# Optimization experiments

Measured on AMD Instinct MI355X. Metric: run time of the kernel, lower is better.

The kernel has to match this reference:

```python
import jax, jax.numpy as jnp
import numpy as np

B, L, K, D = 1024, 8, 16, 64
_KSCALE = 1.0 / np.sqrt(K * D)  # keep channel roughly norm-preserving over layers


def setup_inputs() -> dict:
    key = jax.random.key(0)
    k1, k2, k3, k4 = jax.random.split(key, 4)
    state_re = jax.random.normal(k1, (B, D, D), dtype=jnp.float32)
    state_im = jax.random.normal(k2, (B, D, D), dtype=jnp.float32)
    kraus_re = jax.random.normal(k3, (L, K, D, D), dtype=jnp.float32) * _KSCALE
    kraus_im = jax.random.normal(k4, (L, K, D, D), dtype=jnp.float32) * _KSCALE
    return {"state_re": state_re, "state_im": state_im,
            "kraus_re": kraus_re, "kraus_im": kraus_im}


def reference(state_re, state_im, kraus_re, kraus_im):
    # rho: [B, d, d] complex density matrices; kraus: [L, K, d, d]
    rho = (state_re + 1j * state_im).astype(jnp.complex64)
    kraus = (kraus_re + 1j * kraus_im).astype(jnp.complex64)

    def layer_step(rho, Kl):
        # Kl: [K, d, d]. output_state = sum_k  K_k @ rho @ K_k^dagger
        tmp = jnp.einsum('kij,bjl->kbil', Kl, rho)            # K_k @ rho
        rho_new = jnp.einsum('kbil,kml->bim', tmp, Kl.conj())  # (...) @ K_k^dagger, summed over k
        return rho_new, None

    rho, _ = jax.lax.scan(layer_step, rho, kraus)
    # return real/imag stacked as float32: [2, B, d, d]
    return jnp.stack([rho.real, rho.imag])
```

## Files before the change

### kernel.cpp

```cpp
#include <hip/hip_runtime.h>
#include <hip/hip_fp16.h>

#define D 64
#define NKR 16
#define NB 1024
#define NL 8
#define LSTR 72

typedef __attribute__((ext_vector_type(8))) _Float16 half8;
typedef __attribute__((ext_vector_type(16))) float f32x16;
typedef __attribute__((ext_vector_type(4))) int i32x4;

static __device__ __forceinline__ half8 neg8(half8 x) {
    i32x4 u = __builtin_bit_cast(i32x4, x);
    u = u ^ (int)0x80008000;
    return __builtin_bit_cast(half8, u);
}

union Pack4 { _Float16 h[4]; uint2 u; };

__global__ void kconv_kernel(const float* __restrict__ re, const float* __restrict__ im,
                             _Float16* __restrict__ out) {
    int plane = blockIdx.y;
    int idx = blockIdx.x * blockDim.x + threadIdx.x;
    const float* src = plane ? im : re;
    float4 v = ((const float4*)src)[idx];
    int e = idx * 4;
    int lk = e >> 12;
    int rem = e & 4095;
    Pack4 p;
    p.h[0] = (_Float16)v.x; p.h[1] = (_Float16)v.y;
    p.h[2] = (_Float16)v.z; p.h[3] = (_Float16)v.w;
    *(uint2*)(out + ((size_t)lk * 2 + plane) * 4096 + rem) = p.u;
}

__global__ void sconv_kernel(const float* __restrict__ re, const float* __restrict__ im,
                             _Float16* __restrict__ out) {
    __shared__ float tile[64][65];
    int b = blockIdx.x;
    int t = threadIdx.x;
    for (int plane = 0; plane < 2; ++plane) {
        const float* src = (plane ? im : re) + (size_t)b * 4096;
        __syncthreads();
        #pragma unroll
        for (int i = 0; i < 16; ++i) {
            int e = t + 256 * i;
            tile[e >> 6][e & 63] = src[e];
        }
        __syncthreads();
        _Float16* o = out + ((size_t)b * 2 + plane) * 4096;
        #pragma unroll
        for (int i = 0; i < 16; ++i) {
            int e = t + 256 * i;
            o[e] = (_Float16)tile[e & 63][e >> 6];
        }
    }
}

__global__ __launch_bounds__(256, 4) void layer_kernel(
    const _Float16* __restrict__ rho_in,
    _Float16* __restrict__ rho_out,
    float* __restrict__ final_out,
    const _Float16* __restrict__ kraus,
    int last)
{
    __shared__ __align__(16) _Float16 Klds[2][D][LSTR];
    __shared__ __align__(16) _Float16 Trow[2][D][LSTR];

    const int b    = blockIdx.x;
    const int t    = threadIdx.x;
    const int wv   = t >> 6;
    const int lane = t & 63;
    const int l31  = lane & 31;
    const int hl   = lane >> 5;
    const int wr   = wv >> 1;
    const int wc   = wv & 1;

    half8 a1re[4], a1im[4];
    {
        const _Float16* rb = rho_in + (size_t)b * 2 * D * D;
        const int row = 32 * wr + l31;
        #pragma unroll
        for (int ks = 0; ks < 4; ++ks) {
            const int col = 16 * ks + 8 * hl;
            a1re[ks] = *(const half8*)(rb + row * D + col);
            a1im[ks] = *(const half8*)(rb + D * D + row * D + col);
        }
    }

    f32x16 accRe, accIm;
    #pragma unroll
    for (int i = 0; i < 16; ++i) { accRe[i] = 0.f; accIm[i] = 0.f; }

    #pragma unroll 1
    for (int k = 0; k < NKR; ++k) {
        const uint4* kg = (const uint4*)(kraus + (size_t)k * 2 * D * D);
        #pragma unroll
        for (int r = 0; r < 4; ++r) {
            int idx = t + 256 * r;
            int e0  = idx * 8;
            int plane = e0 >> 12;
            int rem   = e0 & 4095;
            *(uint4*)&Klds[plane][rem >> 6][rem & 63] = kg[idx];
        }
        __syncthreads();

        f32x16 dre, dim;
        #pragma unroll
        for (int i = 0; i < 16; ++i) { dre[i] = 0.f; dim[i] = 0.f; }
        #pragma unroll
        for (int ks = 0; ks < 4; ++ks) {
            const int jcol = 16 * ks + 8 * hl;
            half8 bre  = *(const half8*)&Klds[0][32 * wc + l31][jcol];
            half8 bim  = *(const half8*)&Klds[1][32 * wc + l31][jcol];
            half8 bimn = neg8(bim);
            dre = __builtin_amdgcn_mfma_f32_32x32x16_f16(a1re[ks], bre,  dre, 0, 0, 0);
            dre = __builtin_amdgcn_mfma_f32_32x32x16_f16(a1im[ks], bimn, dre, 0, 0, 0);
            dim = __builtin_amdgcn_mfma_f32_32x32x16_f16(a1re[ks], bim,  dim, 0, 0, 0);
            dim = __builtin_amdgcn_mfma_f32_32x32x16_f16(a1im[ks], bre,  dim, 0, 0, 0);
        }
        {
            const int i = 32 * wc + l31;
            #pragma unroll
            for (int g = 0; g < 4; ++g) {
                Pack4 pr, pi;
                #pragma unroll
                for (int j = 0; j < 4; ++j) {
                    pr.h[j] = (_Float16)dre[4 * g + j];
                    pi.h[j] = (_Float16)dim[4 * g + j];
                }
                const int l0 = 32 * wr + 8 * g + 4 * hl;
                *(uint2*)&Trow[0][i][l0] = pr.u;
                *(uint2*)&Trow[1][i][l0] = pi.u;
            }
        }
        __syncthreads();

        #pragma unroll
        for (int ks = 0; ks < 4; ++ks) {
            const int lcol = 16 * ks + 8 * hl;
            half8 are  = *(const half8*)&Trow[0][32 * wr + l31][lcol];
            half8 aim  = *(const half8*)&Trow[1][32 * wr + l31][lcol];
            half8 bre  = *(const half8*)&Klds[0][32 * wc + l31][lcol];
            half8 bim  = *(const half8*)&Klds[1][32 * wc + l31][lcol];
            half8 bimn = neg8(bim);
            accRe = __builtin_amdgcn_mfma_f32_32x32x16_f16(are, bre,  accRe, 0, 0, 0);
            accRe = __builtin_amdgcn_mfma_f32_32x32x16_f16(aim, bim,  accRe, 0, 0, 0);
            accIm = __builtin_amdgcn_mfma_f32_32x32x16_f16(aim, bre,  accIm, 0, 0, 0);
            accIm = __builtin_amdgcn_mfma_f32_32x32x16_f16(are, bimn, accIm, 0, 0, 0);
        }
        __syncthreads();
    }

    if (!last) {
        _Float16* ob = rho_out + (size_t)b * 2 * D * D;
        const int m = 32 * wc + l31;
        #pragma unroll
        for (int g = 0; g < 4; ++g) {
            Pack4 pr, pi;
            #pragma unroll
            for (int j = 0; j < 4; ++j) {
                pr.h[j] = (_Float16)accRe[4 * g + j];
                pi.h[j] = (_Float16)accIm[4 * g + j];
            }
            const int i0 = 32 * wr + 8 * g + 4 * hl;
            *(uint2*)(ob + m * D + i0)         = pr.u;
            *(uint2*)(ob + D * D + m * D + i0) = pi.u;
        }
    } else {
        float* o0 = final_out + (size_t)b * 4096;
        float* o1 = final_out + (size_t)(NB + b) * 4096;
        const int m = 32 * wc + l31;
        #pragma unroll
        for (int g = 0; g < 4; ++g) {
            #pragma unroll
            for (int j = 0; j < 4; ++j) {
                const int i = 32 * wr + 8 * g + 4 * hl + j;
                o0[i * D + m] = accRe[4 * g + j];
                o1[i * D + m] = accIm[4 * g + j];
            }
        }
    }
}

extern "C" void kernel_launch(void* const* d_in, const int* in_sizes, int n_in,
                              void* d_out, int out_size, void* d_ws, size_t ws_size,
                              hipStream_t stream) {
    const float* state_re = (const float*)d_in[0];
    const float* state_im = (const float*)d_in[1];
    const float* kraus_re = (const float*)d_in[2];
    const float* kraus_im = (const float*)d_in[3];

    _Float16* kraus_h = (_Float16*)d_ws;
    _Float16* bufA = (_Float16*)d_out;
    _Float16* bufB = (_Float16*)((char*)d_out + (size_t)NB * 2 * D * D * sizeof(_Float16));
    float* fout = (float*)d_out;

    kconv_kernel<<<dim3(512, 2), 256, 0, stream>>>(kraus_re, kraus_im, kraus_h);
    sconv_kernel<<<NB, 256, 0, stream>>>(state_re, state_im, bufA);

    for (int l = 0; l < NL; ++l) {
        const _Float16* in = (l & 1) ? bufB : bufA;
        _Float16* out      = (l & 1) ? bufA : bufB;
        layer_kernel<<<NB, 256, 0, stream>>>(in, out, fout,
                                             kraus_h + (size_t)l * NKR * 2 * D * D,
                                             (l == NL - 1) ? 1 : 0);
    }
}
```

Before: 612.3 us.

## Prefetch next Kraus operator via global_load_lds with XOR-swizzled layout

```diff
diff --git a/kernel.cpp b/kernel.cpp
--- a/kernel.cpp
+++ b/kernel.cpp
@@ -18,6 +18,10 @@
 }
 
 union Pack4 { _Float16 h[4]; uint2 u; };
+
+#define GLDS16(gp, lp) \
+    __builtin_amdgcn_global_load_lds((const __attribute__((address_space(1))) void*)(gp), \
+                                     (__attribute__((address_space(3))) void*)(lp), 16, 0, 0)
 
 __global__ void kconv_kernel(const float* __restrict__ re, const float* __restrict__ im,
                              _Float16* __restrict__ out) {
@@ -28,10 +32,12 @@
     int e = idx * 4;
     int lk = e >> 12;
     int rem = e & 4095;
+    int row = rem >> 6, col = rem & 63;
+    int grp = (col >> 3) ^ (row & 7);
     Pack4 p;
     p.h[0] = (_Float16)v.x; p.h[1] = (_Float16)v.y;
     p.h[2] = (_Float16)v.z; p.h[3] = (_Float16)v.w;
-    *(uint2*)(out + ((size_t)lk * 2 + plane) * 4096 + rem) = p.u;
+    *(uint2*)(out + ((size_t)lk * 2 + plane) * 4096 + row * 64 + grp * 8 + (col & 7)) = p.u;
 }
 
 __global__ void sconv_kernel(const float* __restrict__ re, const float* __restrict__ im,
@@ -64,7 +70,7 @@
     const _Float16* __restrict__ kraus,
     int last)
 {
-    __shared__ __align__(16) _Float16 Klds[2][D][LSTR];
+    __shared__ __align__(16) _Float16 Klds[2 * D * D];
     __shared__ __align__(16) _Float16 Trow[2][D][LSTR];
 
     const int b    = blockIdx.x;
@@ -88,66 +94,84 @@
         }
     }
 
+    {
+        const char* kb = (const char*)kraus;
+        const int off = wv * 4096;
+        #pragma unroll
+        for (int r = 0; r < 4; ++r)
+            GLDS16(kb + off + r * 1024 + lane * 16, (char*)Klds + off + r * 1024);
+    }
+
     f32x16 accRe, accIm;
     #pragma unroll
     for (int i = 0; i < 16; ++i) { accRe[i] = 0.f; accIm[i] = 0.f; }
 
+    __syncthreads();
+
+    const int row1  = 32 * wc + l31;
+    const int rb1   = row1 * 64;
+    const int rx1   = row1 & 7;
+
     #pragma unroll 1
     for (int k = 0; k < NKR; ++k) {
-        const uint4* kg = (const uint4*)(kraus + (size_t)k * 2 * D * D);
-        #pragma unroll
-        for (int r = 0; r < 4; ++r) {
-            int idx = t + 256 * r;
-            int e0  = idx * 8;
-            int plane = e0 >> 12;
-            int rem   = e0 & 4095;
-            *(uint4*)&Klds[plane][rem >> 6][rem & 63] = kg[idx];
-        }
-        __syncthreads();
-
-        f32x16 dre, dim;
-        #pragma unroll
-        for (int i = 0; i < 16; ++i) { dre[i] = 0.f; dim[i] = 0.f; }
-        #pragma unroll
-        for (int ks = 0; ks < 4; ++ks) {
-            const int jcol = 16 * ks + 8 * hl;
-            half8 bre  = *(const half8*)&Klds[0][32 * wc + l31][jcol];
-            half8 bim  = *(const half8*)&Klds[1][32 * wc + l31][jcol];
-            half8 bimn = neg8(bim);
-            dre = __builtin_amdgcn_mfma_f32_32x32x16_f16(a1re[ks], bre,  dre, 0, 0, 0);
-            dre = __builtin_amdgcn_mfma_f32_32x32x16_f16(a1im[ks], bimn, dre, 0, 0, 0);
-            dim = __builtin_amdgcn_mfma_f32_32x32x16_f16(a1re[ks], bim,  dim, 0, 0, 0);
-            dim = __builtin_amdgcn_mfma_f32_32x32x16_f16(a1im[ks], bre,  dim, 0, 0, 0);
+        half8 bre[4], bim[4];
+        f32x16 dd;
+        #pragma unroll
+        for (int i = 0; i < 16; ++i) dd[i] = 0.f;
+        #pragma unroll
+        for (int ks = 0; ks < 4; ++ks) {
+            const int g = ((2 * ks + hl) ^ rx1) * 8;
+            bre[ks] = *(const half8*)&Klds[rb1 + g];
+            bim[ks] = *(const half8*)&Klds[4096 + rb1 + g];
+            dd = __builtin_amdgcn_mfma_f32_32x32x16_f16(a1re[ks], bre[ks],       dd, 0, 0, 0);
+            dd = __builtin_amdgcn_mfma_f32_32x32x16_f16(a1im[ks], neg8(bim[ks]), dd, 0, 0, 0);
         }
         {
             const int i = 32 * wc + l31;
             #pragma unroll
             for (int g = 0; g < 4; ++g) {
-                Pack4 pr, pi;
+                Pack4 pr;
                 #pragma unroll
-                for (int j = 0; j < 4; ++j) {
-                    pr.h[j] = (_Float16)dre[4 * g + j];
-                    pi.h[j] = (_Float16)dim[4 * g + j];
-                }
-                const int l0 = 32 * wr + 8 * g + 4 * hl;
-                *(uint2*)&Trow[0][i][l0] = pr.u;
-                *(uint2*)&Trow[1][i][l0] = pi.u;
-            }
-        }
-        __syncthreads();
+                for (int j = 0; j < 4; ++j) pr.h[j] = (_Float16)dd[4 * g + j];
+                *(uint2*)&Trow[0][i][32 * wr + 8 * g + 4 * hl] = pr.u;
+            }
+        }
+        #pragma unroll
+        for (int i = 0; i < 16; ++i) dd[i] = 0.f;
+        #pragma unroll
+        for (int ks = 0; ks < 4; ++ks) {
+            dd = __builtin_amdgcn_mfma_f32_32x32x16_f16(a1re[ks], bim[ks], dd, 0, 0, 0);
+            dd = __builtin_amdgcn_mfma_f32_32x32x16_f16(a1im[ks], bre[ks], dd, 0, 0, 0);
+        }
+        {
+            const int i = 32 * wc + l31;
+            #pragma unroll
+            for (int g = 0; g < 4; ++g) {
+                Pack4 pi;
+                #pragma unroll
+                for (int j = 0; j < 4; ++j) pi.h[j] = (_Float16)dd[4 * g + j];
+                *(uint2*)&Trow[1][i][32 * wr + 8 * g + 4 * hl] = pi.u;
+            }
+        }
+        __syncthreads();
+
+        if (k + 1 < NKR) {
+            const char* kb = (const char*)(kraus + (size_t)(k + 1) * 2 * D * D);
+            const int off = wv * 4096;
+            #pragma unroll
+            for (int r = 0; r < 4; ++r)
+                GLDS16(kb + off + r * 1024 + lane * 16, (char*)Klds + off + r * 1024);
+        }
 
         #pragma unroll
         for (int ks = 0; ks < 4; ++ks) {
             const int lcol = 16 * ks + 8 * hl;
-            half8 are  = *(const half8*)&Trow[0][32 * wr + l31][lcol];
-            half8 aim  = *(const half8*)&Trow[1][32 * wr + l31][lcol];
-            half8 bre  = *(const half8*)&Klds[0][32 * wc + l31][lcol];
-            half8 bim  = *(const half8*)&Klds[1][32 * wc + l31][lcol];
-            half8 bimn = neg8(bim);
-            accRe = __builtin_amdgcn_mfma_f32_32x32x16_f16(are, bre,  accRe, 0, 0, 0);
-            accRe = __builtin_amdgcn_mfma_f32_32x32x16_f16(aim, bim,  accRe, 0, 0, 0);
-            accIm = __builtin_amdgcn_mfma_f32_32x32x16_f16(aim, bre,  accIm, 0, 0, 0);
-            accIm = __builtin_amdgcn_mfma_f32_32x32x16_f16(are, bimn, accIm, 0, 0, 0);
+            half8 are = *(const half8*)&Trow[0][32 * wr + l31][lcol];
+            half8 aim = *(const half8*)&Trow[1][32 * wr + l31][lcol];
+            accRe = __builtin_amdgcn_mfma_f32_32x32x16_f16(are, bre[ks],       accRe, 0, 0, 0);
+            accRe = __builtin_amdgcn_mfma_f32_32x32x16_f16(aim, bim[ks],       accRe, 0, 0, 0);
+            accIm = __builtin_amdgcn_mfma_f32_32x32x16_f16(aim, bre[ks],       accIm, 0, 0, 0);
+            accIm = __builtin_amdgcn_mfma_f32_32x32x16_f16(are, neg8(bim[ks]), accIm, 0, 0, 0);
         }
         __syncthreads();
     }
```

New measurement: 748.7 us. +22.3%, slower.
